# Kernel optimization log

Measured on AMD Instinct MI355X. Metric: run time of the kernel, lower is better.

Reference implementation:

```python
import jax, jax.numpy as jnp
import numpy as np
import math

L, D_T, D, NL, NH, FFN, C, B = 24, 1024, 256, 12, 4, 1024, 2, 2048
HD = D // NH


def _layernorm(x, g, b, eps=1e-5):
    m = jnp.mean(x, axis=-1, keepdims=True)
    v = jnp.mean(jnp.square(x - m), axis=-1, keepdims=True)
    return (x - m) * jax.lax.rsqrt(v + eps) * g + b


def _rotate_half(x):
    x1, x2 = jnp.split(x, 2, axis=-1)
    return jnp.concatenate([-x2, x1], axis=-1)


def setup_inputs() -> dict:
    key = jax.random.key(0)
    ks = iter(jax.random.split(key, 64))
    n = lambda shape, s=0.02: jax.random.normal(next(ks), shape, dtype=jnp.float32) * s
    inp = {}
    inp['teacher_cls'] = jax.random.normal(next(ks), (B, L, D_T), dtype=jnp.float32)
    # input LN + projection
    inp['in_ln_g'] = jnp.ones((D_T,), jnp.float32); inp['in_ln_b'] = jnp.zeros((D_T,), jnp.float32)
    inp['proj_w'] = n((D, D_T)); inp['proj_b'] = jnp.zeros((D,), jnp.float32)
    # RoPE caches (buffers)
    inv_freq = 1.0 / (10000.0 ** (np.arange(0, D, 2, dtype=np.float32) / D))
    t = np.arange(L, dtype=np.float32)
    freqs = np.einsum('i,j->ij', t, inv_freq)
    emb = np.concatenate([freqs, freqs], axis=-1)
    inp['cos_cached'] = jnp.asarray(np.cos(emb)[None])  # [1,L,D]
    inp['sin_cached'] = jnp.asarray(np.sin(emb)[None])
    inp['pre_ln_g'] = jnp.ones((D,), jnp.float32); inp['pre_ln_b'] = jnp.zeros((D,), jnp.float32)
    # stacked transformer layer params [NL, ...]
    inp['l_ln1_g'] = jnp.ones((NL, D), jnp.float32); inp['l_ln1_b'] = jnp.zeros((NL, D), jnp.float32)
    inp['l_inw'] = n((NL, 3 * D, D)); inp['l_inb'] = jnp.zeros((NL, 3 * D), jnp.float32)
    inp['l_outw'] = n((NL, D, D)); inp['l_outb'] = jnp.zeros((NL, D), jnp.float32)
    inp['l_ln2_g'] = jnp.ones((NL, D), jnp.float32); inp['l_ln2_b'] = jnp.zeros((NL, D), jnp.float32)
    inp['l_w12'] = n((NL, 2 * FFN, D)); inp['l_b12'] = jnp.zeros((NL, 2 * FFN), jnp.float32)
    inp['l_w3'] = n((NL, D, FFN)); inp['l_b3'] = jnp.zeros((NL, D), jnp.float32)
    inp['post_ln_g'] = jnp.ones((D,), jnp.float32); inp['post_ln_b'] = jnp.zeros((D,), jnp.float32)
    # entropy gate
    inp['eg_w1'] = n((L, D, 8), 0.01); inp['eg_b1'] = jnp.zeros((L, 8), jnp.float32)
    inp['eg_w2'] = n((L, 8, 1), 0.01); inp['eg_b2'] = jnp.zeros((L, 1), jnp.float32)
    # per-position heads (stacked)
    inp['halt_w'] = n((L, D + 1)); inp['halt_b'] = jnp.full((L,), -4.0, jnp.float32)
    inp['cls_w'] = n((L, C, D)); inp['cls_b'] = jnp.zeros((L, C), jnp.float32)
    return inp


def _mha(x, inw, inb, outw, outb, mask):
    Bb, Ll, Dd = x.shape
    qkv = x @ inw.T + inb                              # [B,L,3D]
    q, k, v = jnp.split(qkv, 3, axis=-1)
    def heads(t):
        return t.reshape(Bb, Ll, NH, HD).transpose(0, 2, 1, 3)  # [B,H,L,hd]
    q, k, v = heads(q), heads(k), heads(v)
    scores = jnp.einsum('bhqd,bhkd->bhqk', q, k) / math.sqrt(HD)
    scores = jnp.where(mask, -jnp.inf, scores)
    attn = jax.nn.softmax(scores, axis=-1)
    o = jnp.einsum('bhqk,bhkd->bhqd', attn, v)
    o = o.transpose(0, 2, 1, 3).reshape(Bb, Ll, Dd)
    return o @ outw.T + outb


def reference(teacher_cls, in_ln_g, in_ln_b, proj_w, proj_b, cos_cached, sin_cached,
              pre_ln_g, pre_ln_b, l_ln1_g, l_ln1_b, l_inw, l_inb, l_outw, l_outb,
              l_ln2_g, l_ln2_b, l_w12, l_b12, l_w3, l_b3, post_ln_g, post_ln_b,
              eg_w1, eg_b1, eg_w2, eg_b2, halt_w, halt_b, cls_w, cls_b):
    x = _layernorm(teacher_cls, in_ln_g, in_ln_b)
    x = x @ proj_w.T + proj_b                          # [B,L,D]
    x = x * cos_cached + _rotate_half(x) * sin_cached  # RoPE
    z = _layernorm(x, pre_ln_g, pre_ln_b)
    mask = jnp.triu(jnp.ones((L, L), bool), 1)         # causal
    for i in range(NL):
        xn = _layernorm(z, l_ln1_g[i], l_ln1_b[i])
        z = z + _mha(xn, l_inw[i], l_inb[i], l_outw[i], l_outb[i], mask)
        xn = _layernorm(z, l_ln2_g[i], l_ln2_b[i])
        w12_out = xn @ l_w12[i].T + l_b12[i]           # [B,L,2*FFN]
        x1, x2 = jnp.split(w12_out, 2, axis=-1)
        hidden = jax.nn.silu(x1) * x2
        z = z + hidden @ l_w3[i].T + l_b3[i]
    z = _layernorm(z, post_ln_g, post_ln_b)
    # batched per-position classifier heads
    class_logits = jnp.einsum('bld,lcd->blc', z, cls_w) + cls_b   # [B,L,C]
    log_probs = jax.nn.log_softmax(class_logits, axis=-1)
    probs = jnp.exp(log_probs)
    probs_safe = jnp.clip(probs, 1e-10, 1.0)
    ent = -jnp.sum(probs_safe * jnp.log(probs_safe), axis=-1, keepdims=True)
    ent_norm = jnp.clip(ent / math.log(C), 0.0, 1.0)              # [B,L,1]
    # entropy gate
    h = jnp.tanh(jnp.einsum('bld,ldh->blh', z, eg_w1) + eg_b1)
    gate = jax.nn.sigmoid(jnp.einsum('blh,lho->blo', h, eg_w2) + eg_b2)
    gated = ent_norm * gate                                        # [B,L,1]
    # batched per-position halting heads
    combined = jnp.concatenate([z, gated], axis=-1)                # [B,L,D+1]
    halting_logits = jnp.einsum('bld,ld->bl', combined, halt_w) + halt_b
    return (halting_logits, class_logits, z)
```

## Files before the change

kernel.cpp:

```cpp
#include <hip/hip_runtime.h>
#include <hip/hip_bf16.h>
#include <math.h>

#define L_SEQ 24
#define DT 1024
#define DM 256
#define NLAYER 12
#define NHEAD 4
#define HDIM 64
#define FFND 1024
#define NCLS 2
#define NBATCH 2048
#define NTOK (NBATCH*L_SEQ)

typedef float f32x4 __attribute__((ext_vector_type(4)));
typedef __bf16 bf16x4 __attribute__((ext_vector_type(4)));
typedef __bf16 bf16x8 __attribute__((ext_vector_type(8)));

#define GLDS16(gp, lp) __builtin_amdgcn_global_load_lds((const __attribute__((address_space(1))) void*)(gp), (__attribute__((address_space(3))) void*)(lp), 16, 0, 0)

__device__ inline float wred_sum(float v){
#pragma unroll
  for (int o = 32; o > 0; o >>= 1) v += __shfl_xor(v, o);
  return v;
}
__device__ inline float wred_max(float v){
#pragma unroll
  for (int o = 32; o > 0; o >>= 1) v = fmaxf(v, __shfl_xor(v, o));
  return v;
}

__device__ __forceinline__ void stageG(const __bf16* __restrict__ gtile, int ldk, int k0,
                                       __bf16* lds_wavebase, int lane, int rowbase){
  int row = rowbase + (lane >> 3);
  int c = (lane & 7) ^ (row & 7);
  GLDS16(gtile + (size_t)row*ldk + k0 + c*8, lds_wavebase);
}

__device__ __forceinline__ bf16x8 ldsfrag(const __bf16* tile, int row, int kk, int lane){
  int c = ((kk << 2) + (lane >> 4)) ^ (row & 7);
  return *(const bf16x8*)(tile + (row << 6) + (c << 3));
}

__global__ void cvt_bf16_kernel(const float* __restrict__ in, __bf16* __restrict__ out, int n4){
  int i = blockIdx.x * blockDim.x + threadIdx.x;
  int stride = gridDim.x * blockDim.x;
  for (; i < n4; i += stride){
    float4 v = ((const float4*)in)[i];
    bf16x4 o;
    o[0] = (__bf16)v.x; o[1] = (__bf16)v.y; o[2] = (__bf16)v.z; o[3] = (__bf16)v.w;
    ((bf16x4*)out)[i] = o;
  }
}

__global__ __launch_bounds__(256) void ln1024_kernel(
    const float* __restrict__ in, const float* __restrict__ g, const float* __restrict__ bb,
    __bf16* __restrict__ out){
  int row = blockIdx.x;
  int tid = threadIdx.x, wid = tid >> 6, lane = tid & 63;
  float4 x = ((const float4*)(in + (size_t)row*DT))[tid];
  float s = x.x + x.y + x.z + x.w;
  float q = x.x*x.x + x.y*x.y + x.z*x.z + x.w*x.w;
  s = wred_sum(s); q = wred_sum(q);
  __shared__ float red[8];
  if (lane == 0){ red[wid] = s; red[4+wid] = q; }
  __syncthreads();
  s = red[0]+red[1]+red[2]+red[3];
  q = red[4]+red[5]+red[6]+red[7];
  float mean = s * (1.f/DT);
  float rstd = rsqrtf(q*(1.f/DT) - mean*mean + 1e-5f);
  float4 gv = ((const float4*)g)[tid], bv = ((const float4*)bb)[tid];
  bf16x4 o;
  o[0] = (__bf16)((x.x-mean)*rstd*gv.x + bv.x);
  o[1] = (__bf16)((x.y-mean)*rstd*gv.y + bv.y);
  o[2] = (__bf16)((x.z-mean)*rstd*gv.z + bv.z);
  o[3] = (__bf16)((x.w-mean)*rstd*gv.w + bv.w);
  ((bf16x4*)(out + (size_t)row*DT))[tid] = o;
}

__global__ __launch_bounds__(256) void rope_preln_kernel(
    float* __restrict__ z, const float* __restrict__ cosc, const float* __restrict__ sinc,
    const float* __restrict__ g, const float* __restrict__ bb,
    const float* __restrict__ g1, const float* __restrict__ b1, __bf16* __restrict__ xnb){
  int row = blockIdx.x*4 + (threadIdx.x >> 6);
  int lane = threadIdx.x & 63;
  int l = row % L_SEQ;
  float4 x = ((const float4*)(z + (size_t)row*DM))[lane];
  float4 p;
  p.x = __shfl_xor(x.x, 32); p.y = __shfl_xor(x.y, 32);
  p.z = __shfl_xor(x.z, 32); p.w = __shfl_xor(x.w, 32);
  float sgn = (lane < 32) ? -1.f : 1.f;
  float4 c = ((const float4*)(cosc + l*DM))[lane];
  float4 sn = ((const float4*)(sinc + l*DM))[lane];
  float4 xr;
  xr.x = x.x*c.x + sgn*p.x*sn.x;
  xr.y = x.y*c.y + sgn*p.y*sn.y;
  xr.z = x.z*c.z + sgn*p.z*sn.z;
  xr.w = x.w*c.w + sgn*p.w*sn.w;
  float s = wred_sum(xr.x + xr.y + xr.z + xr.w);
  float q = wred_sum(xr.x*xr.x + xr.y*xr.y + xr.z*xr.z + xr.w*xr.w);
  float mean = s * (1.f/DM);
  float rstd = rsqrtf(q*(1.f/DM) - mean*mean + 1e-5f);
  float4 gv = ((const float4*)g)[lane], bv = ((const float4*)bb)[lane];
  float4 y;
  y.x = (xr.x-mean)*rstd*gv.x + bv.x;
  y.y = (xr.y-mean)*rstd*gv.y + bv.y;
  y.z = (xr.z-mean)*rstd*gv.z + bv.z;
  y.w = (xr.w-mean)*rstd*gv.w + bv.w;
  ((float4*)(z + (size_t)row*DM))[lane] = y;
  float s2 = wred_sum(y.x + y.y + y.z + y.w);
  float q2 = wred_sum(y.x*y.x + y.y*y.y + y.z*y.z + y.w*y.w);
  float mean2 = s2 * (1.f/DM);
  float rstd2 = rsqrtf(q2*(1.f/DM) - mean2*mean2 + 1e-5f);
  float4 g1v = ((const float4*)g1)[lane], b1v = ((const float4*)b1)[lane];
  bf16x4 o;
  o[0] = (__bf16)((y.x-mean2)*rstd2*g1v.x + b1v.x);
  o[1] = (__bf16)((y.y-mean2)*rstd2*g1v.y + b1v.y);
  o[2] = (__bf16)((y.z-mean2)*rstd2*g1v.z + b1v.z);
  o[3] = (__bf16)((y.w-mean2)*rstd2*g1v.w + b1v.w);
  ((bf16x4*)(xnb + (size_t)row*DM))[lane] = o;
}

template<int MODE, int K>
__global__ __launch_bounds__(512, 2) void gemm512_kernel(
    const __bf16* __restrict__ A, const __bf16* __restrict__ W,
    const float* __restrict__ bias,
    float* __restrict__ Cf, __bf16* __restrict__ Cb,
    int N, int nt){
  __shared__ __align__(16) __bf16 As[256*64];
  __shared__ __align__(16) __bf16 Bs[128*64];
  int bm = blockIdx.x / nt, bn = blockIdx.x % nt;
  int tid = threadIdx.x, wid = tid >> 6, lane = tid & 63;
  int wr = wid >> 1, wc = wid & 1;
  int li = lane & 15, g4 = (lane >> 4) << 2;
  f32x4 acc[4][4] = {};
  const __bf16* ga = A + (size_t)bm*256*K;
  const __bf16* gb = W + (size_t)bn*128*K;
  for (int k0 = 0; k0 < K; k0 += 64){
#pragma unroll
    for (int j = 0; j < 4; j++){ int rb = j*64 + wid*8; stageG(ga, K, k0, As + (rb<<6), lane, rb); }
#pragma unroll
    for (int j = 0; j < 2; j++){ int rb = j*64 + wid*8; stageG(gb, K, k0, Bs + (rb<<6), lane, rb); }
    __syncthreads();
#pragma unroll
    for (int kk = 0; kk < 2; kk++){
      bf16x8 xf[4], wf[4];
#pragma unroll
      for (int mi = 0; mi < 4; mi++) xf[mi] = ldsfrag(As, wr*64 + mi*16 + li, kk, lane);
#pragma unroll
      for (int ni = 0; ni < 4; ni++) wf[ni] = ldsfrag(Bs, wc*64 + ni*16 + li, kk, lane);
#pragma unroll
      for (int ni = 0; ni < 4; ni++)
#pragma unroll
        for (int mi = 0; mi < 4; mi++)
          acc[ni][mi] = __builtin_amdgcn_mfma_f32_16x16x32_bf16(wf[ni], xf[mi], acc[ni][mi], 0, 0, 0);
    }
    __syncthreads();
  }
#pragma unroll
  for (int mi = 0; mi < 4; mi++){
    int m = bm*256 + wr*64 + mi*16 + li;
#pragma unroll
    for (int ni = 0; ni < 4; ni++){
      int n = bn*128 + wc*64 + ni*16 + g4;
      f32x4 bv = *(const f32x4*)(bias + n);
      f32x4 o = acc[ni][mi] + bv;
      if (MODE == 0){
        *(f32x4*)(Cf + (size_t)m*N + n) = o;
      } else {
        bf16x4 ob;
        ob[0] = (__bf16)o[0]; ob[1] = (__bf16)o[1]; ob[2] = (__bf16)o[2]; ob[3] = (__bf16)o[3];
        *(bf16x4*)(Cb + (size_t)m*N + n) = ob;
      }
    }
  }
}

__global__ __launch_bounds__(512, 2) void gemm_glu_kernel(
    const __bf16* __restrict__ A, const __bf16* __restrict__ W12,
    const float* __restrict__ bias, __bf16* __restrict__ H){
  __shared__ __align__(16) __bf16 As[256*64];
  __shared__ __align__(16) __bf16 B1s[128*64];
  __shared__ __align__(16) __bf16 B2s[128*64];
  const int K = 256;
  int bm = blockIdx.x >> 3, bn = blockIdx.x & 7;
  int tid = threadIdx.x, wid = tid >> 6, lane = tid & 63;
  int wr = wid >> 1, wc = wid & 1;
  int li = lane & 15, g4 = (lane >> 4) << 2;
  f32x4 acc1[4][4] = {}, acc2[4][4] = {};
  const __bf16* ga  = A   + (size_t)bm*256*K;
  const __bf16* gb1 = W12 + (size_t)bn*128*K;
  const __bf16* gb2 = gb1 + (size_t)1024*K;
  for (int k0 = 0; k0 < K; k0 += 64){
#pragma unroll
    for (int j = 0; j < 4; j++){ int rb = j*64 + wid*8; stageG(ga,  K, k0, As  + (rb<<6), lane, rb); }
#pragma unroll
    for (int j = 0; j < 2; j++){ int rb = j*64 + wid*8; stageG(gb1, K, k0, B1s + (rb<<6), lane, rb); }
#pragma unroll
    for (int j = 0; j < 2; j++){ int rb = j*64 + wid*8; stageG(gb2, K, k0, B2s + (rb<<6), lane, rb); }
    __syncthreads();
#pragma unroll
    for (int kk = 0; kk < 2; kk++){
      bf16x8 xf[4], w1f[4], w2f[4];
#pragma unroll
      for (int mi = 0; mi < 4; mi++) xf[mi] = ldsfrag(As, wr*64 + mi*16 + li, kk, lane);
#pragma unroll
      for (int ni = 0; ni < 4; ni++){
        w1f[ni] = ldsfrag(B1s, wc*64 + ni*16 + li, kk, lane);
        w2f[ni] = ldsfrag(B2s, wc*64 + ni*16 + li, kk, lane);
      }
#pragma unroll
      for (int ni = 0; ni < 4; ni++)
#pragma unroll
        for (int mi = 0; mi < 4; mi++){
          acc1[ni][mi] = __builtin_amdgcn_mfma_f32_16x16x32_bf16(w1f[ni], xf[mi], acc1[ni][mi], 0, 0, 0);
          acc2[ni][mi] = __builtin_amdgcn_mfma_f32_16x16x32_bf16(w2f[ni], xf[mi], acc2[ni][mi], 0, 0, 0);
        }
    }
    __syncthreads();
  }
#pragma unroll
  for (int mi = 0; mi < 4; mi++){
    int m = bm*256 + wr*64 + mi*16 + li;
#pragma unroll
    for (int ni = 0; ni < 4; ni++){
      int n = bn*128 + wc*64 + ni*16 + g4;
      f32x4 b1v = *(const f32x4*)(bias + n);
      f32x4 b2v = *(const f32x4*)(bias + 1024 + n);
      bf16x4 ob;
#pragma unroll
      for (int r = 0; r < 4; r++){
        float v1 = acc1[ni][mi][r] + b1v[r];
        float v2 = acc2[ni][mi][r] + b2v[r];
        float sig = 1.f/(1.f + __expf(-v1));
        ob[r] = (__bf16)(v1*sig*v2);
      }
      *(bf16x4*)(H + (size_t)m*FFND + n) = ob;
    }
  }
}

template<int K>
__global__ __launch_bounds__(256) void gemm_ln_kernel(
    const __bf16* __restrict__ A, const __bf16* __restrict__ W,
    const float* __restrict__ bias, float* __restrict__ z,
    const float* __restrict__ lng, const float* __restrict__ lnb,
    __bf16* __restrict__ outb, float* __restrict__ outf){
  __shared__ __align__(16) __bf16 As[64*64];
  __shared__ __align__(16) __bf16 Bs[256*64];
  __shared__ float redS[64][4], redQ[64][4];
  int bm = blockIdx.x;
  int wid = threadIdx.x >> 6, lane = threadIdx.x & 63;
  int li = lane & 15, g4 = (lane >> 4) << 2;
  f32x4 acc[4][4] = {};
  const __bf16* ga = A + (size_t)bm*64*K;
  for (int k0 = 0; k0 < K; k0 += 64){
#pragma unroll
    for (int j = 0; j < 2; j++){ int rb = j*32 + wid*8; stageG(ga, K, k0, As + (rb<<6), lane, rb); }
#pragma unroll
    for (int j = 0; j < 8; j++){ int rb = j*32 + wid*8; stageG(W,  K, k0, Bs + (rb<<6), lane, rb); }
    __syncthreads();
#pragma unroll
    for (int kk = 0; kk < 2; kk++){
      bf16x8 xf[4], wf[4];
#pragma unroll
      for (int mi = 0; mi < 4; mi++) xf[mi] = ldsfrag(As, mi*16 + li, kk, lane);
#pragma unroll
      for (int ni = 0; ni < 4; ni++) wf[ni] = ldsfrag(Bs, wid*64 + ni*16 + li, kk, lane);
#pragma unroll
      for (int ni = 0; ni < 4; ni++)
#pragma unroll
        for (int mi = 0; mi < 4; mi++)
          acc[ni][mi] = __builtin_amdgcn_mfma_f32_16x16x32_bf16(wf[ni], xf[mi], acc[ni][mi], 0, 0, 0);
    }
    __syncthreads();
  }
  float sA[4] = {}, qA[4] = {};
#pragma unroll
  for (int mi = 0; mi < 4; mi++){
    int m = bm*64 + mi*16 + li;
#pragma unroll
    for (int ni = 0; ni < 4; ni++){
      int n = wid*64 + ni*16 + g4;
      f32x4 zv = *(const f32x4*)(z + (size_t)m*DM + n);
      f32x4 bv = *(const f32x4*)(bias + n);
      f32x4 v = acc[ni][mi] + bv + zv;
      acc[ni][mi] = v;
      *(f32x4*)(z + (size_t)m*DM + n) = v;
#pragma unroll
      for (int r = 0; r < 4; r++){ sA[mi] += v[r]; qA[mi] += v[r]*v[r]; }
    }
  }
#pragma unroll
  for (int mi = 0; mi < 4; mi++){
    float s = sA[mi], q = qA[mi];
    s += __shfl_xor(s, 16); q += __shfl_xor(q, 16);
    s += __shfl_xor(s, 32); q += __shfl_xor(q, 32);
    if ((lane >> 4) == 0){ redS[mi*16 + li][wid] = s; redQ[mi*16 + li][wid] = q; }
  }
  __syncthreads();
#pragma unroll
  for (int mi = 0; mi < 4; mi++){
    int ml = mi*16 + li;
    float s = redS[ml][0] + redS[ml][1] + redS[ml][2] + redS[ml][3];
    float q = redQ[ml][0] + redQ[ml][1] + redQ[ml][2] + redQ[ml][3];
    float mean = s * (1.f/DM);
    float rstd = rsqrtf(q*(1.f/DM) - mean*mean + 1e-5f);
    int m = bm*64 + ml;
#pragma unroll
    for (int ni = 0; ni < 4; ni++){
      int n = wid*64 + ni*16 + g4;
      f32x4 gv = *(const f32x4*)(lng + n);
      f32x4 bv = *(const f32x4*)(lnb + n);
      if (outb){
        bf16x4 o;
#pragma unroll
        for (int r = 0; r < 4; r++) o[r] = (__bf16)((acc[ni][mi][r] - mean)*rstd*gv[r] + bv[r]);
        *(bf16x4*)(outb + (size_t)m*DM + n) = o;
      } else {
        f32x4 o;
#pragma unroll
        for (int r = 0; r < 4; r++) o[r] = (acc[ni][mi][r] - mean)*rstd*gv[r] + bv[r];
        *(f32x4*)(outf + (size_t)m*DM + n) = o;
      }
    }
  }
}

__global__ __launch_bounds__(256) void attn_kernel(const __bf16* __restrict__ qkv, __bf16* __restrict__ ob){
  int b = blockIdx.x;
  int h = threadIdx.x >> 6, lane = threadIdx.x & 63;
  __shared__ __align__(16) __bf16 Qs[NHEAD][L_SEQ][HDIM];
  __shared__ __align__(16) __bf16 Ks[NHEAD][L_SEQ][HDIM];
  __shared__ float Ps[NHEAD][L_SEQ][L_SEQ];
  const __bf16* base = qkv + (size_t)b*L_SEQ*768;
  float V[L_SEQ];
#pragma unroll
  for (int t = 0; t < L_SEQ; t++){
    int sw = lane ^ ((t & 7) << 3);
    Qs[h][t][sw] = base[t*768 + h*64 + lane];
    Ks[h][t][sw] = base[t*768 + 256 + h*64 + lane];
    V[t] = (float)base[t*768 + 512 + h*64 + lane];
  }
  __syncthreads();
  for (int p = lane; p < L_SEQ*L_SEQ; p += 64){
    int q = p / L_SEQ, k = p - q*L_SEQ;
    if (k <= q){
      int qx = (q & 7) << 3, kx = (k & 7) << 3;
      const __bf16* qr = Qs[h][q];
      const __bf16* kr = Ks[h][k];
      float s = 0.f;
#pragma unroll
      for (int d = 0; d < 64; d += 4){
        bf16x4 qa = *(const bf16x4*)(qr + (d ^ qx));
        bf16x4 ka = *(const bf16x4*)(kr + (d ^ kx));
        s += (float)qa[0]*(float)ka[0] + (float)qa[1]*(float)ka[1]
           + (float)qa[2]*(float)ka[2] + (float)qa[3]*(float)ka[3];
      }
      Ps[h][q][k] = s * 0.125f;
    }
  }
  __syncthreads();
  for (int q = 0; q < L_SEQ; q++){
    float v = (lane <= q) ? Ps[h][q][lane] : -1e30f;
    float mx = wred_max(v);
    float e = (lane <= q) ? __expf(v - mx) : 0.f;
    float sm = wred_sum(e);
    if (lane < L_SEQ) Ps[h][q][lane] = e / sm;
  }
  __syncthreads();
  for (int q = 0; q < L_SEQ; q++){
    float o = 0.f;
    for (int k = 0; k <= q; k++) o += Ps[h][q][k] * V[k];
    ob[((size_t)b*L_SEQ + q)*DM + h*64 + lane] = (__bf16)o;
  }
}

__global__ __launch_bounds__(256) void heads_kernel(
    const float* __restrict__ z,
    const float* __restrict__ cls_w, const float* __restrict__ cls_b,
    const float* __restrict__ eg_w1, const float* __restrict__ eg_b1,
    const float* __restrict__ eg_w2, const float* __restrict__ eg_b2,
    const float* __restrict__ halt_w, const float* __restrict__ halt_b,
    float* __restrict__ halt_out, float* __restrict__ cls_out){
  int m = blockIdx.x*4 + (threadIdx.x >> 6);
  int lane = threadIdx.x & 63;
  int l = m % L_SEQ;
  float4 zv = ((const float4*)(z + (size_t)m*DM))[lane];
  float4 w0 = ((const float4*)(cls_w + ((size_t)l*2 + 0)*DM))[lane];
  float4 w1 = ((const float4*)(cls_w + ((size_t)l*2 + 1)*DM))[lane];
  float c0 = wred_sum(zv.x*w0.x + zv.y*w0.y + zv.z*w0.z + zv.w*w0.w) + cls_b[l*2 + 0];
  float c1 = wred_sum(zv.x*w1.x + zv.y*w1.y + zv.z*w1.z + zv.w*w1.w) + cls_b[l*2 + 1];
  float mx = fmaxf(c0, c1);
  float e0 = __expf(c0 - mx), e1 = __expf(c1 - mx);
  float inv = 1.f/(e0 + e1);
  float p0 = fminf(fmaxf(e0*inv, 1e-10f), 1.f);
  float p1 = fminf(fmaxf(e1*inv, 1e-10f), 1.f);
  float ent = -(p0*__logf(p0) + p1*__logf(p1));
  float entn = fminf(fmaxf(ent * 1.44269504f, 0.f), 1.f);
  const float4* wg = (const float4*)(eg_w1 + ((size_t)l*DM + 4*lane)*8);
  float hacc[8] = {};
#pragma unroll
  for (int dd = 0; dd < 4; dd++){
    float zd = (dd==0) ? zv.x : (dd==1) ? zv.y : (dd==2) ? zv.z : zv.w;
    float4 a = wg[dd*2], b = wg[dd*2 + 1];
    hacc[0] += zd*a.x; hacc[1] += zd*a.y; hacc[2] += zd*a.z; hacc[3] += zd*a.w;
    hacc[4] += zd*b.x; hacc[5] += zd*b.y; hacc[6] += zd*b.z; hacc[7] += zd*b.w;
  }
  float gin = 0.f;
#pragma unroll
  for (int j = 0; j < 8; j++){
    float hj = wred_sum(hacc[j]);
    hj = tanhf(hj + eg_b1[l*8 + j]);
    gin += hj * eg_w2[l*8 + j];
  }
  gin += eg_b2[l];
  float gate = 1.f/(1.f + __expf(-gin));
  float gated = entn * gate;
  const float* hw = halt_w + (size_t)l*257;
  float hp = zv.x*hw[4*lane] + zv.y*hw[4*lane+1] + zv.z*hw[4*lane+2] + zv.w*hw[4*lane+3];
  float hl = wred_sum(hp) + gated*hw[256] + halt_b[l];
  if (lane == 0) halt_out[m] = hl;
  if (lane < 2) cls_out[(size_t)m*2 + lane] = lane ? c1 : c0;
}

extern "C" void kernel_launch(void* const* d_in, const int* in_sizes, int n_in,
                              void* d_out, int out_size, void* d_ws, size_t ws_size,
                              hipStream_t stream){
  const float* teacher = (const float*)d_in[0];
  const float* in_ln_g = (const float*)d_in[1];
  const float* in_ln_b = (const float*)d_in[2];
  const float* proj_w  = (const float*)d_in[3];
  const float* proj_b  = (const float*)d_in[4];
  const float* cosc    = (const float*)d_in[5];
  const float* sinc    = (const float*)d_in[6];
  const float* pre_g   = (const float*)d_in[7];
  const float* pre_b   = (const float*)d_in[8];
  const float* l_ln1_g = (const float*)d_in[9];
  const float* l_ln1_b = (const float*)d_in[10];
  const float* l_inw   = (const float*)d_in[11];
  const float* l_inb   = (const float*)d_in[12];
  const float* l_outw  = (const float*)d_in[13];
  const float* l_outb  = (const float*)d_in[14];
  const float* l_ln2_g = (const float*)d_in[15];
  const float* l_ln2_b = (const float*)d_in[16];
  const float* l_w12   = (const float*)d_in[17];
  const float* l_b12   = (const float*)d_in[18];
  const float* l_w3    = (const float*)d_in[19];
  const float* l_b3    = (const float*)d_in[20];
  const float* post_g  = (const float*)d_in[21];
  const float* post_b  = (const float*)d_in[22];
  const float* eg_w1   = (const float*)d_in[23];
  const float* eg_b1   = (const float*)d_in[24];
  const float* eg_w2   = (const float*)d_in[25];
  const float* eg_b2   = (const float*)d_in[26];
  const float* halt_w  = (const float*)d_in[27];
  const float* halt_b  = (const float*)d_in[28];
  const float* cls_w   = (const float*)d_in[29];
  const float* cls_b   = (const float*)d_in[30];

  float* out = (float*)d_out;
  float* halt_out = out;
  float* cls_out  = out + NTOK;
  float* z_out    = out + NTOK + (size_t)NTOK*NCLS;

  char* ws = (char*)d_ws;
  size_t off = 0;
  auto alloc = [&](size_t bytes){ void* p = ws + off; off += (bytes + 255) & ~(size_t)255; return p; };
  float*  zbuf = (float*) alloc((size_t)NTOK*DM*4);
  __bf16* xnb  = (__bf16*)alloc((size_t)NTOK*DM*2);
  __bf16* qkvb = (__bf16*)alloc((size_t)NTOK*768*2);
  __bf16* obuf = (__bf16*)alloc((size_t)NTOK*DM*2);
  __bf16* bigb = (__bf16*)alloc((size_t)NTOK*1024*2);
  __bf16* w_proj = (__bf16*)alloc((size_t)262144*2);
  __bf16* w_in   = (__bf16*)alloc((size_t)2359296*2);
  __bf16* w_out  = (__bf16*)alloc((size_t)786432*2);
  __bf16* w_12   = (__bf16*)alloc((size_t)6291456*2);
  __bf16* w_3    = (__bf16*)alloc((size_t)3145728*2);

  cvt_bf16_kernel<<<256, 256, 0, stream>>>(proj_w, w_proj, 262144/4);
  cvt_bf16_kernel<<<1024, 256, 0, stream>>>(l_inw, w_in, 2359296/4);
  cvt_bf16_kernel<<<512, 256, 0, stream>>>(l_outw, w_out, 786432/4);
  cvt_bf16_kernel<<<2048, 256, 0, stream>>>(l_w12, w_12, 6291456/4);
  cvt_bf16_kernel<<<1024, 256, 0, stream>>>(l_w3, w_3, 3145728/4);

  ln1024_kernel<<<NTOK, 256, 0, stream>>>(teacher, in_ln_g, in_ln_b, bigb);
  gemm512_kernel<0, 1024><<<192*2, 512, 0, stream>>>(bigb, w_proj, proj_b, zbuf, nullptr, 256, 2);
  rope_preln_kernel<<<NTOK/4, 256, 0, stream>>>(zbuf, cosc, sinc, pre_g, pre_b, l_ln1_g, l_ln1_b, xnb);

  for (int i = 0; i < NLAYER; i++){
    gemm512_kernel<1, 256><<<192*6, 512, 0, stream>>>(xnb, w_in + (size_t)i*768*256, l_inb + i*768, nullptr, qkvb, 768, 6);
    attn_kernel<<<NBATCH, 256, 0, stream>>>(qkvb, obuf);
    gemm_ln_kernel<256><<<NTOK/64, 256, 0, stream>>>(obuf, w_out + (size_t)i*256*256, l_outb + i*256,
                                                     zbuf, l_ln2_g + i*256, l_ln2_b + i*256, xnb, nullptr);
    gemm_glu_kernel<<<192*8, 512, 0, stream>>>(xnb, w_12 + (size_t)i*2048*256, l_b12 + i*2048, bigb);
    bool last = (i == NLAYER-1);
    gemm_ln_kernel<1024><<<NTOK/64, 256, 0, stream>>>(bigb, w_3 + (size_t)i*256*1024, l_b3 + i*256,
                                                      zbuf,
                                                      last ? post_g : l_ln1_g + (i+1)*256,
                                                      last ? post_b : l_ln1_b + (i+1)*256,
                                                      last ? nullptr : xnb,
                                                      last ? z_out : nullptr);
  }

  heads_kernel<<<NTOK/4, 256, 0, stream>>>(z_out, cls_w, cls_b, eg_w1, eg_b1, eg_w2, eg_b2,
                                           halt_w, halt_b, halt_out, cls_out);
}
```

Measured before the change: 4.095 ms.

## Double-buffer GEMM LDS staging with BK=32 tiles and smaller 128x128 blocks

All GEMM kernels now stage K in 32-wide slices into two LDS buffers, issuing the global-to-LDS loads for the next slice while MFMAs run on the current one. A new swizzle matches the 32-column tile layout. The 512-thread, 256-row tiles become 256-thread, 128x128 tiles, which doubles the grid size and can improve occupancy. The cost is one barrier per 32 K-steps instead of two per 64, and each weight tile is reloaded across twice as many M blocks.

```diff
diff --git a/kernel.cpp b/kernel.cpp
--- a/kernel.cpp
+++ b/kernel.cpp
@@ -30,16 +30,15 @@
   return v;
 }
 
-__device__ __forceinline__ void stageG(const __bf16* __restrict__ gtile, int ldk, int k0,
-                                       __bf16* lds_wavebase, int lane, int rowbase){
-  int row = rowbase + (lane >> 3);
-  int c = (lane & 7) ^ (row & 7);
-  GLDS16(gtile + (size_t)row*ldk + k0 + c*8, lds_wavebase);
-}
-
-__device__ __forceinline__ bf16x8 ldsfrag(const __bf16* tile, int row, int kk, int lane){
-  int c = ((kk << 2) + (lane >> 4)) ^ (row & 7);
-  return *(const bf16x8*)(tile + (row << 6) + (c << 3));
+__device__ __forceinline__ void stage16x32(const __bf16* __restrict__ g, int ldk, int k0,
+                                           __bf16* ldsbase, int lane, int rowbase){
+  int r = rowbase + (lane >> 2);
+  int cs = (lane & 3) ^ ((lane >> 3) & 3);
+  GLDS16(g + (size_t)r*ldk + k0 + cs*8, ldsbase);
+}
+__device__ __forceinline__ bf16x8 frag32(const __bf16* tile, int row, int lane){
+  int p = (lane >> 4) ^ ((row >> 1) & 3);
+  return *(const bf16x8*)(tile + (row << 5) + (p << 3));
 }
 
 __global__ void cvt_bf16_kernel(const float* __restrict__ in, __bf16* __restrict__ out, int n4){
@@ -122,44 +121,49 @@
 }
 
 template<int MODE, int K>
-__global__ __launch_bounds__(512, 2) void gemm512_kernel(
+__global__ __launch_bounds__(256) void gemm128_kernel(
     const __bf16* __restrict__ A, const __bf16* __restrict__ W,
     const float* __restrict__ bias,
     float* __restrict__ Cf, __bf16* __restrict__ Cb,
     int N, int nt){
-  __shared__ __align__(16) __bf16 As[256*64];
-  __shared__ __align__(16) __bf16 Bs[128*64];
+  __shared__ __align__(16) __bf16 As[2][128*32];
+  __shared__ __align__(16) __bf16 Bs[2][128*32];
   int bm = blockIdx.x / nt, bn = blockIdx.x % nt;
-  int tid = threadIdx.x, wid = tid >> 6, lane = tid & 63;
+  int wid = threadIdx.x >> 6, lane = threadIdx.x & 63;
   int wr = wid >> 1, wc = wid & 1;
   int li = lane & 15, g4 = (lane >> 4) << 2;
   f32x4 acc[4][4] = {};
-  const __bf16* ga = A + (size_t)bm*256*K;
+  const __bf16* ga = A + (size_t)bm*128*K;
   const __bf16* gb = W + (size_t)bn*128*K;
-  for (int k0 = 0; k0 < K; k0 += 64){
-#pragma unroll
-    for (int j = 0; j < 4; j++){ int rb = j*64 + wid*8; stageG(ga, K, k0, As + (rb<<6), lane, rb); }
-#pragma unroll
-    for (int j = 0; j < 2; j++){ int rb = j*64 + wid*8; stageG(gb, K, k0, Bs + (rb<<6), lane, rb); }
+  const int NT = K/32;
+  auto STAGE = [&](int b, int t){
+    int k0 = t*32;
+    stage16x32(ga, K, k0, &As[b][(wid*32)<<5],      lane, wid*32);
+    stage16x32(ga, K, k0, &As[b][(wid*32+16)<<5],   lane, wid*32+16);
+    stage16x32(gb, K, k0, &Bs[b][(wid*32)<<5],      lane, wid*32);
+    stage16x32(gb, K, k0, &Bs[b][(wid*32+16)<<5],   lane, wid*32+16);
+  };
+  STAGE(0, 0);
+  __syncthreads();
+  int cur = 0;
+  for (int t = 0; t < NT; t++){
+    if (t + 1 < NT) STAGE(cur^1, t+1);
+    bf16x8 xf[4], wf[4];
+#pragma unroll
+    for (int mi = 0; mi < 4; mi++) xf[mi] = frag32(As[cur], wr*64 + mi*16 + li, lane);
+#pragma unroll
+    for (int ni = 0; ni < 4; ni++) wf[ni] = frag32(Bs[cur], wc*64 + ni*16 + li, lane);
+#pragma unroll
+    for (int ni = 0; ni < 4; ni++)
+#pragma unroll
+      for (int mi = 0; mi < 4; mi++)
+        acc[ni][mi] = __builtin_amdgcn_mfma_f32_16x16x32_bf16(wf[ni], xf[mi], acc[ni][mi], 0, 0, 0);
     __syncthreads();
-#pragma unroll
-    for (int kk = 0; kk < 2; kk++){
-      bf16x8 xf[4], wf[4];
-#pragma unroll
-      for (int mi = 0; mi < 4; mi++) xf[mi] = ldsfrag(As, wr*64 + mi*16 + li, kk, lane);
-#pragma unroll
-      for (int ni = 0; ni < 4; ni++) wf[ni] = ldsfrag(Bs, wc*64 + ni*16 + li, kk, lane);
-#pragma unroll
-      for (int ni = 0; ni < 4; ni++)
-#pragma unroll
-        for (int mi = 0; mi < 4; mi++)
-          acc[ni][mi] = __builtin_amdgcn_mfma_f32_16x16x32_bf16(wf[ni], xf[mi], acc[ni][mi], 0, 0, 0);
-    }
-    __syncthreads();
+    cur ^= 1;
   }
 #pragma unroll
   for (int mi = 0; mi < 4; mi++){
-    int m = bm*256 + wr*64 + mi*16 + li;
+    int m = bm*128 + wr*64 + mi*16 + li;
 #pragma unroll
     for (int ni = 0; ni < 4; ni++){
       int n = bn*128 + wc*64 + ni*16 + g4;
@@ -176,52 +180,56 @@
   }
 }
 
-__global__ __launch_bounds__(512, 2) void gemm_glu_kernel(
+__global__ __launch_bounds__(256) void gemm_glu_kernel(
     const __bf16* __restrict__ A, const __bf16* __restrict__ W12,
     const float* __restrict__ bias, __bf16* __restrict__ H){
-  __shared__ __align__(16) __bf16 As[256*64];
-  __shared__ __align__(16) __bf16 B1s[128*64];
-  __shared__ __align__(16) __bf16 B2s[128*64];
+  __shared__ __align__(16) __bf16 As[2][128*32];
+  __shared__ __align__(16) __bf16 B1s[2][128*32];
+  __shared__ __align__(16) __bf16 B2s[2][128*32];
   const int K = 256;
   int bm = blockIdx.x >> 3, bn = blockIdx.x & 7;
-  int tid = threadIdx.x, wid = tid >> 6, lane = tid & 63;
+  int wid = threadIdx.x >> 6, lane = threadIdx.x & 63;
   int wr = wid >> 1, wc = wid & 1;
   int li = lane & 15, g4 = (lane >> 4) << 2;
   f32x4 acc1[4][4] = {}, acc2[4][4] = {};
-  const __bf16* ga  = A   + (size_t)bm*256*K;
+  const __bf16* ga  = A   + (size_t)bm*128*K;
   const __bf16* gb1 = W12 + (size_t)bn*128*K;
   const __bf16* gb2 = gb1 + (size_t)1024*K;
-  for (int k0 = 0; k0 < K; k0 += 64){
-#pragma unroll
-    for (int j = 0; j < 4; j++){ int rb = j*64 + wid*8; stageG(ga,  K, k0, As  + (rb<<6), lane, rb); }
-#pragma unroll
-    for (int j = 0; j < 2; j++){ int rb = j*64 + wid*8; stageG(gb1, K, k0, B1s + (rb<<6), lane, rb); }
-#pragma unroll
-    for (int j = 0; j < 2; j++){ int rb = j*64 + wid*8; stageG(gb2, K, k0, B2s + (rb<<6), lane, rb); }
+  auto STAGE = [&](int b, int t){
+    int k0 = t*32;
+    stage16x32(ga,  K, k0, &As[b][(wid*32)<<5],     lane, wid*32);
+    stage16x32(ga,  K, k0, &As[b][(wid*32+16)<<5],  lane, wid*32+16);
+    stage16x32(gb1, K, k0, &B1s[b][(wid*32)<<5],    lane, wid*32);
+    stage16x32(gb1, K, k0, &B1s[b][(wid*32+16)<<5], lane, wid*32+16);
+    stage16x32(gb2, K, k0, &B2s[b][(wid*32)<<5],    lane, wid*32);
+    stage16x32(gb2, K, k0, &B2s[b][(wid*32+16)<<5], lane, wid*32+16);
+  };
+  STAGE(0, 0);
+  __syncthreads();
+  int cur = 0;
+  for (int t = 0; t < 8; t++){
+    if (t < 7) STAGE(cur^1, t+1);
+    bf16x8 xf[4], w1f[4], w2f[4];
+#pragma unroll
+    for (int mi = 0; mi < 4; mi++) xf[mi] = frag32(As[cur], wr*64 + mi*16 + li, lane);
+#pragma unroll
+    for (int ni = 0; ni < 4; ni++){
+      w1f[ni] = frag32(B1s[cur], wc*64 + ni*16 + li, lane);
+      w2f[ni] = frag32(B2s[cur], wc*64 + ni*16 + li, lane);
+    }
+#pragma unroll
+    for (int ni = 0; ni < 4; ni++)
+#pragma unroll
+      for (int mi = 0; mi < 4; mi++){
+        acc1[ni][mi] = __builtin_amdgcn_mfma_f32_16x16x32_bf16(w1f[ni], xf[mi], acc1[ni][mi], 0, 0, 0);
+        acc2[ni][mi] = __builtin_amdgcn_mfma_f32_16x16x32_bf16(w2f[ni], xf[mi], acc2[ni][mi], 0, 0, 0);
+      }
     __syncthreads();
-#pragma unroll
-    for (int kk = 0; kk < 2; kk++){
-      bf16x8 xf[4], w1f[4], w2f[4];
-#pragma unroll
-      for (int mi = 0; mi < 4; mi++) xf[mi] = ldsfrag(As, wr*64 + mi*16 + li, kk, lane);
-#pragma unroll
-      for (int ni = 0; ni < 4; ni++){
-        w1f[ni] = ldsfrag(B1s, wc*64 + ni*16 + li, kk, lane);
-        w2f[ni] = ldsfrag(B2s, wc*64 + ni*16 + li, kk, lane);
-      }
-#pragma unroll
-      for (int ni = 0; ni < 4; ni++)
-#pragma unroll
-        for (int mi = 0; mi < 4; mi++){
-          acc1[ni][mi] = __builtin_amdgcn_mfma_f32_16x16x32_bf16(w1f[ni], xf[mi], acc1[ni][mi], 0, 0, 0);
-          acc2[ni][mi] = __builtin_amdgcn_mfma_f32_16x16x32_bf16(w2f[ni], xf[mi], acc2[ni][mi], 0, 0, 0);
-        }
-    }
-    __syncthreads();
+    cur ^= 1;
   }
 #pragma unroll
   for (int mi = 0; mi < 4; mi++){
-    int m = bm*256 + wr*64 + mi*16 + li;
+    int m = bm*128 + wr*64 + mi*16 + li;
 #pragma unroll
     for (int ni = 0; ni < 4; ni++){
       int n = bn*128 + wc*64 + ni*16 + g4;
@@ -246,34 +254,39 @@
     const float* __restrict__ bias, float* __restrict__ z,
     const float* __restrict__ lng, const float* __restrict__ lnb,
     __bf16* __restrict__ outb, float* __restrict__ outf){
-  __shared__ __align__(16) __bf16 As[64*64];
-  __shared__ __align__(16) __bf16 Bs[256*64];
+  __shared__ __align__(16) __bf16 As[2][64*32];
+  __shared__ __align__(16) __bf16 Bs[2][256*32];
   __shared__ float redS[64][4], redQ[64][4];
   int bm = blockIdx.x;
   int wid = threadIdx.x >> 6, lane = threadIdx.x & 63;
   int li = lane & 15, g4 = (lane >> 4) << 2;
   f32x4 acc[4][4] = {};
   const __bf16* ga = A + (size_t)bm*64*K;
-  for (int k0 = 0; k0 < K; k0 += 64){
-#pragma unroll
-    for (int j = 0; j < 2; j++){ int rb = j*32 + wid*8; stageG(ga, K, k0, As + (rb<<6), lane, rb); }
-#pragma unroll
-    for (int j = 0; j < 8; j++){ int rb = j*32 + wid*8; stageG(W,  K, k0, Bs + (rb<<6), lane, rb); }
+  const int NT = K/32;
+  auto STAGE = [&](int b, int t){
+    int k0 = t*32;
+    stage16x32(ga, K, k0, &As[b][(wid*16)<<5], lane, wid*16);
+#pragma unroll
+    for (int j = 0; j < 4; j++)
+      stage16x32(W, K, k0, &Bs[b][(wid*64 + j*16)<<5], lane, wid*64 + j*16);
+  };
+  STAGE(0, 0);
+  __syncthreads();
+  int cur = 0;
+  for (int t = 0; t < NT; t++){
+    if (t + 1 < NT) STAGE(cur^1, t+1);
+    bf16x8 xf[4], wf[4];
+#pragma unroll
+    for (int mi = 0; mi < 4; mi++) xf[mi] = frag32(As[cur], mi*16 + li, lane);
+#pragma unroll
+    for (int ni = 0; ni < 4; ni++) wf[ni] = frag32(Bs[cur], wid*64 + ni*16 + li, lane);
+#pragma unroll
+    for (int ni = 0; ni < 4; ni++)
+#pragma unroll
+      for (int mi = 0; mi < 4; mi++)
+        acc[ni][mi] = __builtin_amdgcn_mfma_f32_16x16x32_bf16(wf[ni], xf[mi], acc[ni][mi], 0, 0, 0);
     __syncthreads();
-#pragma unroll
-    for (int kk = 0; kk < 2; kk++){
-      bf16x8 xf[4], wf[4];
-#pragma unroll
-      for (int mi = 0; mi < 4; mi++) xf[mi] = ldsfrag(As, mi*16 + li, kk, lane);
-#pragma unroll
-      for (int ni = 0; ni < 4; ni++) wf[ni] = ldsfrag(Bs, wid*64 + ni*16 + li, kk, lane);
-#pragma unroll
-      for (int ni = 0; ni < 4; ni++)
-#pragma unroll
-        for (int mi = 0; mi < 4; mi++)
-          acc[ni][mi] = __builtin_amdgcn_mfma_f32_16x16x32_bf16(wf[ni], xf[mi], acc[ni][mi], 0, 0, 0);
-    }
-    __syncthreads();
+    cur ^= 1;
   }
   float sA[4] = {}, qA[4] = {};
 #pragma unroll
@@ -485,15 +498,15 @@
   cvt_bf16_kernel<<<1024, 256, 0, stream>>>(l_w3, w_3, 3145728/4);
 
   ln1024_kernel<<<NTOK, 256, 0, stream>>>(teacher, in_ln_g, in_ln_b, bigb);
-  gemm512_kernel<0, 1024><<<192*2, 512, 0, stream>>>(bigb, w_proj, proj_b, zbuf, nullptr, 256, 2);
+  gemm128_kernel<0, 1024><<<384*2, 256, 0, stream>>>(bigb, w_proj, proj_b, zbuf, nullptr, 256, 2);
   rope_preln_kernel<<<NTOK/4, 256, 0, stream>>>(zbuf, cosc, sinc, pre_g, pre_b, l_ln1_g, l_ln1_b, xnb);
 
   for (int i = 0; i < NLAYER; i++){
-    gemm512_kernel<1, 256><<<192*6, 512, 0, stream>>>(xnb, w_in + (size_t)i*768*256, l_inb + i*768, nullptr, qkvb, 768, 6);
+    gemm128_kernel<1, 256><<<384*6, 256, 0, stream>>>(xnb, w_in + (size_t)i*768*256, l_inb + i*768, nullptr, qkvb, 768, 6);
     attn_kernel<<<NBATCH, 256, 0, stream>>>(qkvb, obuf);
     gemm_ln_kernel<256><<<NTOK/64, 256, 0, stream>>>(obuf, w_out + (size_t)i*256*256, l_outb + i*256,
                                                      zbuf, l_ln2_g + i*256, l_ln2_b + i*256, xnb, nullptr);
-    gemm_glu_kernel<<<192*8, 512, 0, stream>>>(xnb, w_12 + (size_t)i*2048*256, l_b12 + i*2048, bigb);
+    gemm_glu_kernel<<<384*8, 256, 0, stream>>>(xnb, w_12 + (size_t)i*2048*256, l_b12 + i*2048, bigb);
     bool last = (i == NLAYER-1);
     gemm_ln_kernel<1024><<<NTOK/64, 256, 0, stream>>>(bigb, w_3 + (size_t)i*256*1024, l_b3 + i*256,
                                                       zbuf,
```

Result: slower. 4.517 ms (+10.3%).
